# Performance work log

Hardware: AMD Instinct MI355X
Metric: run time of the kernel (lower is better)

Reference implementation:

```python
import jax, jax.numpy as jnp
import numpy as np

NUM_HEADS = 16
FUTURE_FRAMES = 2
DIM = 1024


def setup_inputs() -> dict:
    key = jax.random.key(0)
    kx, kqkv, kp, kb = jax.random.split(key, 4)
    B, T = 2, 2048
    x = jax.random.normal(kx, (B, T, DIM), dtype=jnp.float32)
    # torch Linear weights stored transposed for direct x @ W use
    w_qkv = jax.random.normal(kqkv, (DIM, 3 * DIM), dtype=jnp.float32) * (DIM ** -0.5)
    w_proj = jax.random.normal(kp, (DIM, DIM), dtype=jnp.float32) * (DIM ** -0.5)
    b_proj = jax.random.normal(kb, (DIM,), dtype=jnp.float32) * 0.01
    return {"x": x, "w_qkv": w_qkv, "w_proj": w_proj, "b_proj": b_proj}


def reference(x, w_qkv, w_proj, b_proj):
    B, T, dim = x.shape
    H = NUM_HEADS
    hd = dim // H
    qkv = x @ w_qkv                                    # (B, T, 3*dim)
    q, k, v = jnp.split(qkv, 3, axis=-1)
    # (B, H, T, hd)
    q = q.reshape(B, T, H, hd).transpose(0, 2, 1, 3)
    k = k.reshape(B, T, H, hd).transpose(0, 2, 1, 3)
    v = v.reshape(B, T, H, hd).transpose(0, 2, 1, 3)
    scale = hd ** -0.5
    scores = jnp.einsum('bhqd,bhkd->bhqk', q, k) * scale
    # banded mask: query i may attend keys j with i <= j <= i + future_frames
    i = jnp.arange(T)[:, None]
    j = jnp.arange(T)[None, :]
    allowed = (j >= i) & (j <= i + FUTURE_FRAMES)       # (T, T)
    scores = jnp.where(allowed[None, None], scores, -jnp.inf)
    attn = jax.nn.softmax(scores, axis=-1)
    out = jnp.einsum('bhqk,bhkd->bhqd', attn, v)        # (B, H, T, hd)
    out = out.transpose(0, 2, 1, 3).reshape(B, T, dim)
    return out @ w_proj + b_proj
```

## Files before the change

kernel.cpp:

```cpp
#include <hip/hip_runtime.h>
#include <hip/hip_bf16.h>
#include <cstdint>
#include <cstddef>

#define T_SEQ 2048
#define NBATCH 2
#define DIMSZ 1024
#define NHEAD 16
#define HDIM 64

typedef float f32x4 __attribute__((ext_vector_type(4)));
typedef short bf16x8 __attribute__((ext_vector_type(8)));

__device__ __forceinline__ void gld_lds16(const __hip_bfloat16* g, __hip_bfloat16* l) {
    __builtin_amdgcn_global_load_lds(
        (const __attribute__((address_space(1))) unsigned int*)g,
        (__attribute__((address_space(3))) unsigned int*)l,
        16, 0, 0);
}

__device__ __forceinline__ float bf2f(unsigned short u) {
    union { unsigned int i; float f; } c; c.i = (unsigned int)u << 16; return c.f;
}

__global__ __launch_bounds__(256) void prep(
    const float* __restrict__ x,      __hip_bfloat16* __restrict__ xb,
    const float* __restrict__ wqkv,   __hip_bfloat16* __restrict__ wqkvT,
    const float* __restrict__ wproj,  __hip_bfloat16* __restrict__ wprojT)
{
    __shared__ float tile[32][33];
    const int b = blockIdx.x;
    if (b < 4096) {
        int i = (b * 256 + threadIdx.x) * 4;
        float4 v = *(const float4*)(x + i);
        union { __hip_bfloat16 h[4]; ushort4 u; } pk;
        pk.h[0] = __hip_bfloat16(v.x); pk.h[1] = __hip_bfloat16(v.y);
        pk.h[2] = __hip_bfloat16(v.z); pk.h[3] = __hip_bfloat16(v.w);
        *(ushort4*)(xb + i) = pk.u;
        return;
    }
    const float* in; __hip_bfloat16* out; int C, c0, r0;
    if (b < 7168) {
        int bb = b - 4096; in = wqkv; out = wqkvT; C = 3072;
        c0 = (bb % 96) * 32; r0 = (bb / 96) * 32;
    } else {
        int bb = b - 7168; in = wproj; out = wprojT; C = 1024;
        c0 = (bb & 31) * 32; r0 = (bb >> 5) * 32;
    }
    const int tx = threadIdx.x & 31, ty = threadIdx.x >> 5;
#pragma unroll
    for (int p = 0; p < 32; p += 8)
        tile[ty + p][tx] = in[(size_t)(r0 + ty + p) * C + c0 + tx];
    __syncthreads();
#pragma unroll
    for (int p = 0; p < 32; p += 8)
        out[(size_t)(c0 + ty + p) * 1024 + r0 + tx] = __hip_bfloat16(tile[tx][ty + p]);
}

#define BAR() do { asm volatile("" ::: "memory"); __builtin_amdgcn_s_barrier(); \
                   asm volatile("" ::: "memory"); } while (0)

#define STAGE1(G, S, rb, kt)                                                   \
    do {                                                                       \
        _Pragma("unroll")                                                      \
        for (int s_ = 0; s_ < 2; ++s_) {                                       \
            int row_ = s_ * 128 + (tid >> 2);                                  \
            int cbg_ = scb ^ (((row_ >> 1) & 3) << 4);                        \
            gld_lds16(G + (size_t)row_ * K + (kt) * 32 + (cbg_ >> 1),          \
                      &S[rb][row_ * 32 + (scb >> 1)]);                         \
        }                                                                      \
    } while (0)

__global__ __launch_bounds__(512, 2) void gemm256_ring(
    const __hip_bfloat16* __restrict__ A,
    const __hip_bfloat16* __restrict__ Bt,
    __hip_bfloat16* __restrict__ C,
    int M, int N, int K)
{
    __shared__ __align__(16) __hip_bfloat16 As[4][256 * 32];
    __shared__ __align__(16) __hip_bfloat16 Bs[4][256 * 32];

    const int tid  = threadIdx.x;
    const int lane = tid & 63;
    const int wv   = tid >> 6;
    const int wm   = wv >> 2;
    const int wn   = wv & 3;

    const int nwg = gridDim.x;
    const int cpx = nwg >> 3;
    const int bid = blockIdx.x;
    const int swb = (bid & 7) * cpx + (bid >> 3);
    const int nbn = N >> 8;
    const int bm = swb / nbn, bn = swb % nbn;

    const int NT = K >> 5;

    const __hip_bfloat16* Ag = A  + (size_t)(bm << 8) * K;
    const __hip_bfloat16* Bg = Bt + (size_t)(bn << 8) * K;

    const int scb = (tid & 3) << 4;

    const int fm = lane & 15;
    const int fq = (lane >> 4) << 3;

    f32x4 acc[8][4] = {};

    STAGE1(Ag, As, 0, 0); STAGE1(Bg, Bs, 0, 0);
    STAGE1(Ag, As, 1, 1); STAGE1(Bg, Bs, 1, 1);
    STAGE1(Ag, As, 2, 2); STAGE1(Bg, Bs, 2, 2);

    for (int s = 0; s < NT; ++s) {
        int kt3 = s + 3; if (kt3 >= NT) kt3 -= NT;
        const int rcur = s & 3;
        const int rnxt = kt3 & 3;

        STAGE1(Ag, As, rnxt, kt3);
        STAGE1(Bg, Bs, rnxt, kt3);

        asm volatile("s_waitcnt vmcnt(12)" ::: "memory");
        BAR();

        bf16x8 af[8], bfv[4];
#pragma unroll
        for (int i = 0; i < 8; ++i) {
            int row_ = wm * 128 + i * 16 + fm;
            int ce_  = fq ^ (((row_ >> 1) & 3) << 3);
            af[i] = *(const bf16x8*)&As[rcur][row_ * 32 + ce_];
        }
#pragma unroll
        for (int j = 0; j < 4; ++j) {
            int row_ = wn * 64 + j * 16 + fm;
            int ce_  = fq ^ (((row_ >> 1) & 3) << 3);
            bfv[j] = *(const bf16x8*)&Bs[rcur][row_ * 32 + ce_];
        }

        __builtin_amdgcn_sched_barrier(0);
        __builtin_amdgcn_s_setprio(1);
#pragma unroll
        for (int i = 0; i < 8; ++i)
#pragma unroll
            for (int j = 0; j < 4; ++j)
                acc[i][j] = __builtin_amdgcn_mfma_f32_16x16x32_bf16(
                    af[i], bfv[j], acc[i][j], 0, 0, 0);
        __builtin_amdgcn_s_setprio(0);
        __builtin_amdgcn_sched_barrier(0);
        BAR();
    }
    asm volatile("s_waitcnt vmcnt(0)" ::: "memory");

    const int fcol  = lane & 15;
    const int frow4 = (lane >> 4) << 2;
    const int cm0 = (bm << 8) + wm * 128;
    const int cn0 = (bn << 8) + wn * 64;
#pragma unroll
    for (int nj = 0; nj < 4; ++nj) {
        int col = cn0 + nj * 16 + fcol;
#pragma unroll
        for (int mi = 0; mi < 8; ++mi)
#pragma unroll
            for (int r = 0; r < 4; ++r) {
                int row = cm0 + mi * 16 + frow4 + r;
                C[(size_t)row * N + col] = __hip_bfloat16(acc[mi][nj][r]);
            }
    }
}

__global__ __launch_bounds__(256) void gemm_bt_64(
    const __hip_bfloat16* __restrict__ A,
    const __hip_bfloat16* __restrict__ Bt,
    const float* __restrict__ bias,
    float* __restrict__ C,
    int M, int N, int K)
{
    __shared__ __align__(16) __hip_bfloat16 As2[2 * 64 * 32];
    __shared__ __align__(16) __hip_bfloat16 Bs2[2 * 128 * 32];

    const int tid  = threadIdx.x;
    const int wv   = tid >> 6;
    const int lane = tid & 63;
    const int bn   = blockIdx.x, bm = blockIdx.y;
    const int wm   = wv >> 1, wn = wv & 1;

    f32x4 acc[2][4] = {};

    const int srow = lane >> 2;
    const int scol = (lane & 3) * 8;

    const __hip_bfloat16* Ag = A  + (size_t)(bm * 64) * K;
    const __hip_bfloat16* Bg = Bt + (size_t)(bn * 128) * K;

    const int fm = lane & 15;
    const int fq = (lane >> 4) * 8;

    for (int kk = 0; kk < K; kk += 64) {
#pragma unroll
        for (int kh = 0; kh < 2; ++kh) {
            {
                int row = wv * 16 + srow;
                gld_lds16(Ag + (size_t)row * K + kk + kh * 32 + scol,
                          As2 + kh * 2048 + row * 32 + scol);
            }
#pragma unroll
            for (int it = 0; it < 2; ++it) {
                int row = (it * 4 + wv) * 16 + srow;
                gld_lds16(Bg + (size_t)row * K + kk + kh * 32 + scol,
                          Bs2 + kh * 4096 + row * 32 + scol);
            }
        }
        __syncthreads();

#pragma unroll
        for (int kh = 0; kh < 2; ++kh) {
            bf16x8 af[2], bfr[4];
#pragma unroll
            for (int i = 0; i < 2; ++i)
                af[i] = *(const bf16x8*)(As2 + kh * 2048 + (wm * 32 + i * 16 + fm) * 32 + fq);
#pragma unroll
            for (int j = 0; j < 4; ++j)
                bfr[j] = *(const bf16x8*)(Bs2 + kh * 4096 + (wn * 64 + j * 16 + fm) * 32 + fq);
#pragma unroll
            for (int i = 0; i < 2; ++i)
#pragma unroll
                for (int j = 0; j < 4; ++j)
                    acc[i][j] = __builtin_amdgcn_mfma_f32_16x16x32_bf16(af[i], bfr[j], acc[i][j], 0, 0, 0);
        }
        __syncthreads();
    }

    const int fcol  = lane & 15;
    const int frow4 = (lane >> 4) * 4;
    const int cm0 = bm * 64 + wm * 32;
    const int cn0 = bn * 128 + wn * 64;
#pragma unroll
    for (int j = 0; j < 4; ++j) {
        int col = cn0 + j * 16 + fcol;
        float bv = bias[col];
#pragma unroll
        for (int i = 0; i < 2; ++i)
#pragma unroll
            for (int r = 0; r < 4; ++r) {
                int row = cm0 + i * 16 + frow4 + r;
                C[(size_t)row * N + col] = acc[i][j][r] + bv;
            }
    }
}

__global__ __launch_bounds__(256) void attn_banded(
    const __hip_bfloat16* __restrict__ qkv,
    __hip_bfloat16* __restrict__ o)
{
    const int t4 = threadIdx.x;
    const int r  = blockIdx.x;
    const int t  = r & (T_SEQ - 1);
    const size_t rb = (size_t)r * (3 * DIMSZ);
    const int d0 = t4 * 4;

    ushort4 qu = *(const ushort4*)(qkv + rb + d0);
    float q0 = bf2f(qu.x), q1 = bf2f(qu.y), q2 = bf2f(qu.z), q3 = bf2f(qu.w);

    float s[3], vvx[3], vvy[3], vvz[3], vvw[3];
#pragma unroll
    for (int j = 0; j < 3; ++j) {
        bool ok = (t + j) < T_SEQ;
        size_t rbj = ok ? rb + (size_t)j * (3 * DIMSZ) : rb;
        ushort4 ku = *(const ushort4*)(qkv + rbj + DIMSZ + d0);
        ushort4 vu = *(const ushort4*)(qkv + rbj + 2 * DIMSZ + d0);
        vvx[j] = bf2f(vu.x); vvy[j] = bf2f(vu.y); vvz[j] = bf2f(vu.z); vvw[j] = bf2f(vu.w);
        float d = q0 * bf2f(ku.x) + q1 * bf2f(ku.y) + q2 * bf2f(ku.z) + q3 * bf2f(ku.w);
#pragma unroll
        for (int off = 8; off > 0; off >>= 1)
            d += __shfl_xor(d, off, 64);
        s[j] = ok ? d * 0.125f : -1e30f;
    }
    float m  = fmaxf(s[0], fmaxf(s[1], s[2]));
    float p0 = __expf(s[0] - m), p1 = __expf(s[1] - m), p2 = __expf(s[2] - m);
    float inv = 1.0f / (p0 + p1 + p2);
    union { __hip_bfloat16 h[4]; ushort4 uu; } pk;
    pk.h[0] = __hip_bfloat16((p0 * vvx[0] + p1 * vvx[1] + p2 * vvx[2]) * inv);
    pk.h[1] = __hip_bfloat16((p0 * vvy[0] + p1 * vvy[1] + p2 * vvy[2]) * inv);
    pk.h[2] = __hip_bfloat16((p0 * vvz[0] + p1 * vvz[1] + p2 * vvz[2]) * inv);
    pk.h[3] = __hip_bfloat16((p0 * vvw[0] + p1 * vvw[1] + p2 * vvw[2]) * inv);
    *(ushort4*)(o + (size_t)r * DIMSZ + d0) = pk.uu;
}

extern "C" void kernel_launch(void* const* d_in, const int* in_sizes, int n_in,
                              void* d_out, int out_size, void* d_ws, size_t ws_size,
                              hipStream_t stream) {
    const float* x      = (const float*)d_in[0];
    const float* w_qkv  = (const float*)d_in[1];
    const float* w_proj = (const float*)d_in[2];
    const float* b_proj = (const float*)d_in[3];
    float* out = (float*)d_out;

    const int M = NBATCH * T_SEQ;

    char* ws = (char*)d_ws;
    __hip_bfloat16* xb     = (__hip_bfloat16*)(ws);
    __hip_bfloat16* attn   = (__hip_bfloat16*)(ws);
    __hip_bfloat16* wqkvT  = (__hip_bfloat16*)(ws + (8u  << 20));
    __hip_bfloat16* wprojT = (__hip_bfloat16*)(ws + (14u << 20));
    __hip_bfloat16* qkv    = (__hip_bfloat16*)(ws + (16u << 20));

    prep<<<8192, 256, 0, stream>>>(x, xb, w_qkv, wqkvT, w_proj, wprojT);

    gemm256_ring<<<dim3((M / 256) * (3 * DIMSZ / 256)), 512, 0, stream>>>(
        xb, wqkvT, qkv, M, 3 * DIMSZ, DIMSZ);

    attn_banded<<<M, 256, 0, stream>>>(qkv, attn);

    gemm_bt_64<<<dim3(DIMSZ / 128, M / 64), 256, 0, stream>>>(
        attn, wprojT, b_proj, out, M, DIMSZ, DIMSZ);
}
```

Before: 157.4 us.

## Restructure QKV GEMM into four-phase quadrant pipeline with 64-wide K tiles

```diff
diff --git a/kernel.cpp b/kernel.cpp
--- a/kernel.cpp
+++ b/kernel.cpp
@@ -59,32 +59,77 @@
 
 #define BAR() do { asm volatile("" ::: "memory"); __builtin_amdgcn_s_barrier(); \
                    asm volatile("" ::: "memory"); } while (0)
-
-#define STAGE1(G, S, rb, kt)                                                   \
-    do {                                                                       \
-        _Pragma("unroll")                                                      \
-        for (int s_ = 0; s_ < 2; ++s_) {                                       \
-            int row_ = s_ * 128 + (tid >> 2);                                  \
-            int cbg_ = scb ^ (((row_ >> 1) & 3) << 4);                        \
-            gld_lds16(G + (size_t)row_ * K + (kt) * 32 + (cbg_ >> 1),          \
-                      &S[rb][row_ * 32 + (scb >> 1)]);                         \
-        }                                                                      \
+#define LGKM0_SB() do { asm volatile("s_waitcnt lgkmcnt(0)" ::: "memory"); \
+                        __builtin_amdgcn_sched_barrier(0); } while (0)
+#define VM10() asm volatile("s_waitcnt vmcnt(10)" ::: "memory")
+
+#define STAGEH(G, Sdst, kt, h)                                                  \
+    do {                                                                        \
+        _Pragma("unroll")                                                       \
+        for (int s_ = 0; s_ < 2; ++s_) {                                        \
+            int lr_ = s_ * 64 + (tid >> 3);                                     \
+            int gu_ = (tid & 7) ^ (lr_ & 7);                                    \
+            gld_lds16(G + (size_t)((h) * 128 + lr_) * K + (kt) * 64 + gu_ * 8,  \
+                      (Sdst) + lr_ * 64 + (tid & 7) * 8);                       \
+        }                                                                       \
     } while (0)
 
-__global__ __launch_bounds__(512, 2) void gemm256_ring(
+#define READ_A(buf, qi)                                                         \
+    do {                                                                        \
+        _Pragma("unroll")                                                       \
+        for (int i_ = 0; i_ < 4; ++i_) {                                        \
+            int lr_ = wq2 * 64 + i_ * 16 + fm;                                  \
+            _Pragma("unroll")                                                   \
+            for (int kh_ = 0; kh_ < 2; ++kh_) {                                 \
+                int u_ = (kh_ * 4 + fu) ^ (lr_ & 7);                            \
+                a[i_][kh_] = *(const bf16x8*)&As[buf][qi][lr_ * 64 + u_ * 8];   \
+            }                                                                   \
+        }                                                                       \
+    } while (0)
+
+#define READ_B(buf, qj, dst)                                                    \
+    do {                                                                        \
+        _Pragma("unroll")                                                       \
+        for (int j_ = 0; j_ < 2; ++j_) {                                        \
+            int lr_ = wq4 * 32 + j_ * 16 + fm;                                  \
+            _Pragma("unroll")                                                   \
+            for (int kh_ = 0; kh_ < 2; ++kh_) {                                 \
+                int u_ = (kh_ * 4 + fu) ^ (lr_ & 7);                            \
+                dst[j_][kh_] = *(const bf16x8*)&Bs[buf][qj][lr_ * 64 + u_ * 8]; \
+            }                                                                   \
+        }                                                                       \
+    } while (0)
+
+#define MFMA16(QI, QJ, bsrc)                                                    \
+    do {                                                                        \
+        __builtin_amdgcn_s_setprio(1);                                          \
+        _Pragma("unroll")                                                       \
+        for (int i_ = 0; i_ < 4; ++i_)                                          \
+            _Pragma("unroll")                                                   \
+            for (int j_ = 0; j_ < 2; ++j_)                                      \
+                _Pragma("unroll")                                               \
+                for (int kh_ = 0; kh_ < 2; ++kh_)                               \
+                    acc[QI][QJ][i_][j_] =                                       \
+                        __builtin_amdgcn_mfma_f32_16x16x32_bf16(                \
+                            a[i_][kh_], bsrc[j_][kh_],                          \
+                            acc[QI][QJ][i_][j_], 0, 0, 0);                      \
+        __builtin_amdgcn_s_setprio(0);                                          \
+    } while (0)
+
+__global__ __launch_bounds__(512, 2) void gemm256_4ph(
     const __hip_bfloat16* __restrict__ A,
     const __hip_bfloat16* __restrict__ Bt,
     __hip_bfloat16* __restrict__ C,
     int M, int N, int K)
 {
-    __shared__ __align__(16) __hip_bfloat16 As[4][256 * 32];
-    __shared__ __align__(16) __hip_bfloat16 Bs[4][256 * 32];
+    __shared__ __align__(16) __hip_bfloat16 As[2][2][128 * 64];
+    __shared__ __align__(16) __hip_bfloat16 Bs[2][2][128 * 64];
 
     const int tid  = threadIdx.x;
     const int lane = tid & 63;
     const int wv   = tid >> 6;
-    const int wm   = wv >> 2;
-    const int wn   = wv & 3;
+    const int wq2  = wv >> 2;
+    const int wq4  = wv & 3;
 
     const int nwg = gridDim.x;
     const int cpx = nwg >> 3;
@@ -93,76 +138,77 @@
     const int nbn = N >> 8;
     const int bm = swb / nbn, bn = swb % nbn;
 
-    const int NT = K >> 5;
+    const int NT = K >> 6;
 
     const __hip_bfloat16* Ag = A  + (size_t)(bm << 8) * K;
     const __hip_bfloat16* Bg = Bt + (size_t)(bn << 8) * K;
 
-    const int scb = (tid & 3) << 4;
-
     const int fm = lane & 15;
-    const int fq = (lane >> 4) << 3;
-
-    f32x4 acc[8][4] = {};
-
-    STAGE1(Ag, As, 0, 0); STAGE1(Bg, Bs, 0, 0);
-    STAGE1(Ag, As, 1, 1); STAGE1(Bg, Bs, 1, 1);
-    STAGE1(Ag, As, 2, 2); STAGE1(Bg, Bs, 2, 2);
-
-    for (int s = 0; s < NT; ++s) {
-        int kt3 = s + 3; if (kt3 >= NT) kt3 -= NT;
-        const int rcur = s & 3;
-        const int rnxt = kt3 & 3;
-
-        STAGE1(Ag, As, rnxt, kt3);
-        STAGE1(Bg, Bs, rnxt, kt3);
-
-        asm volatile("s_waitcnt vmcnt(12)" ::: "memory");
+    const int fu = lane >> 4;
+
+    f32x4 acc[2][2][4][2] = {};
+    bf16x8 a[4][2], b0[2][2], b1[2][2];
+
+    STAGEH(Ag, &As[0][0][0], 0, 0);
+    STAGEH(Bg, &Bs[0][0][0], 0, 0);
+    STAGEH(Bg, &Bs[0][1][0], 0, 1);
+    STAGEH(Ag, &As[0][1][0], 0, 1);
+    STAGEH(Ag, &As[1][0][0], 1, 0);
+    STAGEH(Bg, &Bs[1][0][0], 1, 0);
+    STAGEH(Bg, &Bs[1][1][0], 1, 1);
+    VM10();
+    BAR();
+
+    for (int t = 0; t < NT; ++t) {
+        const int cur = t & 1, nxt = cur ^ 1;
+        int t1 = t + 1; if (t1 >= NT) t1 -= NT;
+        int t2 = t + 2; if (t2 >= NT) t2 -= NT;
+
+        READ_A(cur, 0);
+        READ_B(cur, 0, b0);
+        STAGEH(Ag, &As[nxt][1][0], t1, 1);
+        BAR(); LGKM0_SB();
+        MFMA16(0, 0, b0);
+        VM10();
         BAR();
 
-        bf16x8 af[8], bfv[4];
-#pragma unroll
-        for (int i = 0; i < 8; ++i) {
-            int row_ = wm * 128 + i * 16 + fm;
-            int ce_  = fq ^ (((row_ >> 1) & 3) << 3);
-            af[i] = *(const bf16x8*)&As[rcur][row_ * 32 + ce_];
-        }
-#pragma unroll
-        for (int j = 0; j < 4; ++j) {
-            int row_ = wn * 64 + j * 16 + fm;
-            int ce_  = fq ^ (((row_ >> 1) & 3) << 3);
-            bfv[j] = *(const bf16x8*)&Bs[rcur][row_ * 32 + ce_];
-        }
-
-        __builtin_amdgcn_sched_barrier(0);
-        __builtin_amdgcn_s_setprio(1);
-#pragma unroll
-        for (int i = 0; i < 8; ++i)
-#pragma unroll
-            for (int j = 0; j < 4; ++j)
-                acc[i][j] = __builtin_amdgcn_mfma_f32_16x16x32_bf16(
-                    af[i], bfv[j], acc[i][j], 0, 0, 0);
-        __builtin_amdgcn_s_setprio(0);
-        __builtin_amdgcn_sched_barrier(0);
+        READ_B(cur, 1, b1);
+        STAGEH(Ag, &As[cur][0][0], t2, 0);
+        BAR(); LGKM0_SB();
+        MFMA16(0, 1, b1);
+        VM10();
+        BAR();
+
+        READ_A(cur, 1);
+        STAGEH(Bg, &Bs[cur][0][0], t2, 0);
+        BAR(); LGKM0_SB();
+        MFMA16(1, 0, b0);
+        BAR();
+
+        STAGEH(Bg, &Bs[cur][1][0], t2, 1);
+        MFMA16(1, 1, b1);
+        VM10();
         BAR();
     }
     asm volatile("s_waitcnt vmcnt(0)" ::: "memory");
 
     const int fcol  = lane & 15;
     const int frow4 = (lane >> 4) << 2;
-    const int cm0 = (bm << 8) + wm * 128;
-    const int cn0 = (bn << 8) + wn * 64;
-#pragma unroll
-    for (int nj = 0; nj < 4; ++nj) {
-        int col = cn0 + nj * 16 + fcol;
-#pragma unroll
-        for (int mi = 0; mi < 8; ++mi)
-#pragma unroll
-            for (int r = 0; r < 4; ++r) {
-                int row = cm0 + mi * 16 + frow4 + r;
-                C[(size_t)row * N + col] = __hip_bfloat16(acc[mi][nj][r]);
+#pragma unroll
+    for (int qi = 0; qi < 2; ++qi)
+#pragma unroll
+        for (int qj = 0; qj < 2; ++qj)
+#pragma unroll
+            for (int j = 0; j < 2; ++j) {
+                int col = (bn << 8) + qj * 128 + wq4 * 32 + j * 16 + fcol;
+#pragma unroll
+                for (int i = 0; i < 4; ++i)
+#pragma unroll
+                    for (int r = 0; r < 4; ++r) {
+                        int row = (bm << 8) + qi * 128 + wq2 * 64 + i * 16 + frow4 + r;
+                        C[(size_t)row * N + col] = __hip_bfloat16(acc[qi][qj][i][j][r]);
+                    }
             }
-    }
 }
 
 __global__ __launch_bounds__(256) void gemm_bt_64(
@@ -303,7 +349,7 @@
 
     prep<<<8192, 256, 0, stream>>>(x, xb, w_qkv, wqkvT, w_proj, wprojT);
 
-    gemm256_ring<<<dim3((M / 256) * (3 * DIMSZ / 256)), 512, 0, stream>>>(
+    gemm256_4ph<<<dim3((M / 256) * (3 * DIMSZ / 256)), 512, 0, stream>>>(
         xb, wqkvT, qkv, M, 3 * DIMSZ, DIMSZ);
 
     attn_banded<<<M, 256, 0, stream>>>(qkv, attn);
```

Result: faster. 150.2 us (-4.6%).
